# Kernel optimization log

Measured on AMD Instinct MI355X. Metric: run time of the kernel, lower is better.

The kernel has to match this reference:

```python
import jax, jax.numpy as jnp
import numpy as np
import math

B, T = 8, 16
CODE_NUM = 1024
CODE_SIZE = 48
GRAPH_SIZE = 32
HIDDEN = 150      # hidden_size == t_output_size
T_ATTN = 32       # t_attention_size
DP_ATTN = 32      # DotProductAttention size
OUT = 1024


def _lin(k, fan_in, fan_out):
    s = 1.0 / math.sqrt(fan_in)
    kw, kb = jax.random.split(k)
    W = jax.random.uniform(kw, (fan_in, fan_out), minval=-s, maxval=s, dtype=jnp.float32)
    b = jax.random.uniform(kb, (fan_out,), minval=-s, maxval=s, dtype=jnp.float32)
    return W, b


def setup_inputs():
    key = jax.random.key(0)
    ks = jax.random.split(key, 16)
    u = jax.random.uniform(ks[0], (B, T, CODE_NUM))
    m1 = (u < 0.03).astype(jnp.float32)                   # persistent codes
    m2 = ((u >= 0.03) & (u < 0.05)).astype(jnp.float32)   # emerging neighbor codes
    m3 = ((u >= 0.05) & (u < 0.06)).astype(jnp.float32)   # emerging unrelated codes
    divided = jnp.stack([m1, m2, m3], axis=-1)            # [B,T,N,3], disjoint
    code_x = jnp.clip(m1 + m2 + m3, 0.0, 1.0)             # current-visit codes
    neighbors = ((u >= 0.06) & (u < 0.12)).astype(jnp.float32)
    lens = jax.random.randint(ks[1], (B,), T // 2, T + 1)
    a = (jax.random.uniform(ks[2], (CODE_NUM, CODE_NUM)) < 0.01).astype(jnp.float32)
    adj = a / (a.sum(axis=1, keepdims=True) + 1e-6)
    c_emb = jax.random.normal(ks[3], (CODE_NUM, CODE_SIZE)) * 0.05
    n_emb = jax.random.normal(ks[4], (CODE_NUM, CODE_SIZE)) * 0.05
    u_emb = jax.random.normal(ks[5], (CODE_NUM, GRAPH_SIZE)) * 0.05
    Wg, bg = _lin(ks[6], CODE_SIZE, GRAPH_SIZE)           # GraphLayer dense
    Wi, bi = _lin(ks[7], GRAPH_SIZE, 3 * HIDDEN)          # GRUCell input (r|z|n)
    Wh, bh = _lin(ks[8], HIDDEN, 3 * HIDDEN)              # GRUCell hidden (r|z|n)
    Wq, bq = _lin(ks[9], GRAPH_SIZE, T_ATTN)
    Wk, bk = _lin(ks[10], GRAPH_SIZE, T_ATTN)
    Wv, bv = _lin(ks[11], GRAPH_SIZE, HIDDEN)
    Wd, bd = _lin(ks[12], HIDDEN, DP_ATTN)                # DotProductAttention dense
    context = jax.random.normal(ks[13], (DP_ATTN,)) * 0.1
    Wc, bc = _lin(ks[14], HIDDEN, OUT)                    # Classifier
    return dict(code_x=code_x, divided=divided, neighbors=neighbors, lens=lens,
                adj=adj, c_emb=c_emb, n_emb=n_emb, u_emb=u_emb, Wg=Wg, bg=bg,
                Wi=Wi, bi=bi, Wh=Wh, bh=bh, Wq=Wq, bq=bq, Wk=Wk, bk=bk,
                Wv=Wv, bv=bv, Wd=Wd, bd=bd, context=context, Wc=Wc, bc=bc)


def _forward(code_x, divided, neighbors, lens, adj, c_emb, n_emb, u_emb,
             Wg, bg, Wi, bi, Wh, bh, Wq, bq, Wk, bk, Wv, bv, Wd, bd, context, Wc, bc):
    Bb, Tt, N = code_x.shape
    H = Wh.shape[0]
    NEG = -1e30
    scale = 1.0 / math.sqrt(Wq.shape[1])

    def step(carry, xs):
        h_prev, no_prev = carry                 # [B,N,H], [B,N,G]
        c_t, d_t, n_t, t_idx = xs               # [B,N], [B,N,3], [B,N], scalar
        c = c_t[..., None]
        nb = n_t[..., None]
        # GraphLayer: masked embeddings + one-hop adjacency aggregation
        ce = c * c_emb                           # [B,N,C]
        ne = nb * n_emb
        adj_ce = jnp.einsum('mn,bnc->bmc', adj, ce)
        adj_ne = jnp.einsum('mn,bnc->bmc', adj, ne)
        co = jax.nn.leaky_relu((ce + c * adj_ce + c * adj_ne) @ Wg + bg)      # [B,N,G]
        no = jax.nn.leaky_relu((ne + nb * adj_ne + nb * adj_ce) @ Wg + bg)

        m1 = d_t[..., 0]; m2 = d_t[..., 1]; m3 = d_t[..., 2]
        # TransitionLayer part 1: GRUCell on persistent (m1) codes; h_new starts at 0
        gi = co @ Wi + bi
        gh = h_prev @ Wh + bh
        i_r, i_z, i_n = jnp.split(gi, 3, axis=-1)
        h_r, h_z, h_n = jnp.split(gh, 3, axis=-1)
        r = jax.nn.sigmoid(i_r + h_r)
        z = jax.nn.sigmoid(i_z + h_z)
        n_g = jnp.tanh(i_n + r * h_n)
        h_m1 = (1.0 - z) * n_g + z * h_prev
        h_new = jnp.where(m1[..., None] > 0, h_m1, 0.0)

        # TransitionLayer part 2: single-head attention over emerging (m2|m3) codes, t>0
        m23 = (m2 + m3) > 0
        qrows = jnp.where(m2[..., None] > 0, no_prev,
                          jnp.where(m3[..., None] > 0, u_emb, 0.0))           # [B,N,G]
        q = qrows @ Wq + bq
        k = co @ Wk + bk
        v = qrows @ Wv + bv
        s = jnp.einsum('bia,bja->bij', q, k) * scale
        s = jnp.where(m23[:, None, :], s, NEG)   # keys restricted to m2|m3 set
        h_m23 = jnp.tanh(jnp.einsum('bij,bjh->bih', jax.nn.softmax(s, axis=-1), v))
        use23 = t_idx > 0
        h_new = jnp.where(jnp.logical_and(use23, m23)[..., None], h_m23, h_new)

        # per-step output: max-pool over each active subset (0 if subset empty)
        om1 = jnp.max(jnp.where(m1[..., None] > 0, h_m1, NEG), axis=1)
        om1 = jnp.where(jnp.any(m1 > 0, axis=1)[:, None], om1, 0.0)
        om23 = jnp.max(jnp.where(m23[..., None], h_m23, NEG), axis=1)
        om23 = jnp.where(jnp.logical_and(use23, jnp.any(m23, axis=1))[:, None], om23, 0.0)
        return (h_new, no), om1 + om23

    h0 = jnp.zeros((Bb, N, H), code_x.dtype)
    no0 = jnp.zeros((Bb, N, Wg.shape[1]), code_x.dtype)
    xs = (jnp.moveaxis(code_x, 1, 0), jnp.moveaxis(divided, 1, 0),
          jnp.moveaxis(neighbors, 1, 0), jnp.arange(Tt))
    _, outs = jax.lax.scan(step, (h0, no0), xs)
    outs = jnp.moveaxis(outs, 0, 1)              # [B,T,H]

    # DotProductAttention over (ragged) visit axis
    vu = (outs @ Wd + bd) @ context              # [B,T]
    tmask = jnp.arange(Tt)[None, :] < lens[:, None]
    score = jax.nn.softmax(jnp.where(tmask, vu, NEG), axis=-1)
    pooled = jnp.einsum('bth,bt->bh', outs, score)
    # Classifier (dropout_rate=0 -> identity) with sigmoid activation
    return jax.nn.sigmoid(pooled @ Wc + bc)


def reference(code_x, divided, neighbors, lens, adj, c_emb, n_emb, u_emb,
              Wg, bg, Wi, bi, Wh, bh, Wq, bq, Wk, bk, Wv, bv, Wd, bd, context, Wc, bc):
    return _forward(code_x, divided, neighbors, lens, adj, c_emb, n_emb, u_emb,
                    Wg, bg, Wi, bi, Wh, bh, Wq, bq, Wk, bk, Wv, bv, Wd, bd,
                    context, Wc, bc)
```

## Files before the change

### kernel.cpp

```cpp
#include <hip/hip_runtime.h>

#define Bq   8
#define Tq   16
#define Nq   1024
#define Cq   48
#define Gq   32
#define Hq   150
#define H3q  450
#define TAq  32
#define OUTq 1024
#define BTq  128
#define NBLK (2 * BTq)

#define NC_CAP 128
#define NM_CAP 64
#define NACT   (2 * NC_CAP)
#define MTILE  16
#define NMH    (NM_CAP / 2)

__device__ __forceinline__ float lrelu(float x){ return x > 0.f ? x : 0.01f * x; }
__device__ __forceinline__ float sigm(float x){ return 1.f / (1.f + expf(-x)); }

__device__ int   g_n1[BTq], g_n23[BTq], g_nchain[BTq], g_nchain2[BTq];
__device__ int   g_list1[BTq][NM_CAP];
__device__ int   g_list23[BTq][NM_CAP];
__device__ int   g_mapc[BTq][Nq];
__device__ int   g_mapn[BTq][Nq];
__device__ int   g_chain[BTq][NM_CAP];
__device__ int   g_chain2[BTq][NM_CAP];
__device__ int   g_cls[BTq][NM_CAP];
__device__ float g_co[BTq][NC_CAP][Gq];
__device__ float g_no[BTq][NC_CAP][Gq];
__device__ float g_hm23[BTq][NM_CAP][Hq];
__device__ float g_om23p2[2][BTq][Hq];
__device__ float g_hm1[BTq][NM_CAP][Hq];
__device__ float g_om1p2[2][BTq][Hq];
__device__ float g_om1c[BTq][Hq];

template<typename T>
__device__ __forceinline__ T gld(const T* p){
    return __hip_atomic_load(p, __ATOMIC_RELAXED, __HIP_MEMORY_SCOPE_AGENT);
}
template<typename T>
__device__ __forceinline__ void gst(T* p, T v){
    __hip_atomic_store(p, v, __ATOMIC_RELAXED, __HIP_MEMORY_SCOPE_AGENT);
}

__device__ unsigned int g_done[NBLK][16];

__device__ __forceinline__ void publish(unsigned int val){
    asm volatile("s_waitcnt vmcnt(0)" ::: "memory");
    __syncthreads();
    if (threadIdx.x == 0)
        __hip_atomic_store(&g_done[blockIdx.x][0], val,
                           __ATOMIC_RELAXED, __HIP_MEMORY_SCOPE_AGENT);
}

__device__ __forceinline__ void spin_ge(int b2, unsigned int tgt){
    while ((int)(__hip_atomic_load(&g_done[b2][0],
                                   __ATOMIC_RELAXED, __HIP_MEMORY_SCOPE_AGENT) - tgt) < 0)
        __builtin_amdgcn_s_sleep(4);
}

__device__ __forceinline__ void gi3(const float* co_row, const float* Wi, const float* bi, int h,
                                    float& gr, float& gz, float& gn){
    gr = bi[h]; gz = bi[Hq + h]; gn = bi[2 * Hq + h];
    #pragma unroll
    for (int g = 0; g < Gq; ++g){
        float c = co_row[g];
        const float* w = Wi + g * H3q + h;
        gr += c * w[0];
        gz += c * w[Hq];
        gn += c * w[2 * Hq];
    }
}

#define WARM(ptr, nfloats) { int nv_ = (nfloats) >> 2; \
    for (int i4_ = blk * 512 + tid; i4_ < nv_; i4_ += NBLK * 512){ \
        float4 v_ = ((const float4*)(ptr))[i4_]; \
        wacc += v_.x + v_.y + v_.z + v_.w; } }

union SharedU {
    struct {
        unsigned char cf[Nq], nf[Nq];
        short lc[NC_CAP], ln[NC_CAP];
        short act[NACT];
        float Wg[Cq][Gq];
        float Pact[NACT][Gq];
        float A[MTILE][NACT];
    } co;
    struct {
        unsigned char f1[Nq], f2[Nq], f3[Nq];
        short l1[NM_CAP], l23[NM_CAP];
        unsigned char wm[NMH];
        float co23[NM_CAP][Gq];
        float qr[NM_CAP][Gq];
        float q[NMH][TAq + 1];
        float k[NM_CAP][TAq + 1];
        float s[NMH][NM_CAP + 1];
        float vv[NM_CAP][Hq];
        float hm[NMH][Hq];
    } mid;
    struct {
        short map1p[Nq], map23p[Nq];
        short l1[NM_CAP];
        unsigned char cls[NM_CAP];
        int   m23l[NM_CAP];
        float co1[NMH][Gq];
        float hb[Hq];
        float ghf[H3q];
        float gi[NMH][H3q];
    } g1;
    struct {
        unsigned char defer[NM_CAP];
        float co[Gq];
        float hb[Hq];
        float ghf[H3q];
        float cmax[Hq];
    } g1b;
    struct {
        int   nch2[Tq];
        float co[Gq];
        float hb[Hq];
        float ghf[H3q];
        float outs[Tq][Hq];
        float wdc[Hq];
        float score[Tq];
        float pooled[Hq];
    } fin;
};

#define CO_PREFETCH(P, kk) { int rbase_ = half + (kk) * 2 * MTILE; \
    int ntile_ = min(MTILE, (total - rbase_ + 1) / 2); int lim_ = ntile_ * total; \
    _Pragma("unroll") for (int u = 0; u < 8; ++u){ int idx_ = tid + u * 512; \
        if (idx_ < lim_){ int ti_ = idx_ / total, j_ = idx_ - ti_ * total; \
            P[u] = adj[(size_t)sh.co.act[rbase_ + 2 * ti_] * Nq + sh.co.act[j_]]; } } }

#define CO_STORE(P, kk) { int rbase_ = half + (kk) * 2 * MTILE; \
    int ntile_ = min(MTILE, (total - rbase_ + 1) / 2); int lim_ = ntile_ * total; \
    _Pragma("unroll") for (int u = 0; u < 8; ++u){ int idx_ = tid + u * 512; \
        if (idx_ < lim_){ int ti_ = idx_ / total, j_ = idx_ - ti_ * total; \
            sh.co.A[ti_][j_] = P[u]; } } }

#define CO_COMPUTE(kk) { int rbase_ = half + (kk) * 2 * MTILE; \
    int ntile_ = min(MTILE, (total - rbase_ + 1) / 2); \
    if (grp < ntile_){ int r_ = rbase_ + 2 * grp; float agg_ = 0.f; \
        _Pragma("unroll 4") for (int j_ = 0; j_ < total; ++j_) \
            agg_ += sh.co.A[grp][j_] * sh.co.Pact[j_][g]; \
        float v_ = lrelu(sh.co.Pact[r_][g] + agg_ + bgv); \
        if (r_ < nc) gst(&g_co[bt][r_][g], v_); else gst(&g_no[bt][r_ - nc][g], v_); } }

__global__ __launch_bounds__(512, 1) void k_fused(
    const float* code_x, const float* divided, const float* neighbors,
    const int* lens, const float* adj, const float* c_emb, const float* n_emb,
    const float* u_emb, const float* Wg, const float* bg,
    const float* Wi, const float* bi, const float* Wh, const float* bh,
    const float* Wq_, const float* bq_, const float* Wk_, const float* bk_,
    const float* Wv_, const float* bv_, const float* Wd, const float* bd,
    const float* ctx, const float* Wc, const float* bc, float* out)
{
    __shared__ SharedU sh;
    __shared__ int s_n0, s_n1v, s_i2;
    const int tid = threadIdx.x;
    const int blk = blockIdx.x;
    const int bt   = blk >> 1;
    const int half = blk & 1;
    const int t    = bt % Tq;
    const int btp  = bt - 1;
    const unsigned int bar0 = __hip_atomic_load(&g_done[blk][0],
                                                __ATOMIC_RELAXED, __HIP_MEMORY_SCOPE_AGENT);

    float wacc = 0.f;
    WARM(adj,     Nq * Nq);
    WARM(divided, BTq * Nq * 3);
    WARM(c_emb,   Nq * Cq);
    WARM(n_emb,   Nq * Cq);
    WARM(u_emb,   Nq * Gq);
    WARM(Wi,      Gq * H3q);
    WARM(Wh,      Hq * H3q);
    WARM(Wc,      Hq * OUTq);
    WARM(Wv_,     Gq * Hq);
    WARM(Wd,      Hq * TAq);

    {
        int wave = tid >> 6, lane = tid & 63;
        for (int n = tid; n < Nq; n += 512){
            sh.co.cf[n] = (code_x[bt * Nq + n]    > 0.f) ? 1 : 0;
            sh.co.nf[n] = (neighbors[bt * Nq + n] > 0.f) ? 1 : 0;
        }
        for (int i = tid; i < Cq * Gq; i += 512) (&sh.co.Wg[0][0])[i] = Wg[i];
        __syncthreads();
        if (wave == 0){
            int base = 0;
            for (int start = 0; start < Nq; start += 64){
                int n = start + lane;
                int pred = sh.co.cf[n];
                unsigned long long mm = __ballot(pred != 0);
                int pos = base + (int)__popcll(mm & ((1ull << lane) - 1ull));
                if (pred && pos < NC_CAP) sh.co.lc[pos] = (short)n;
                base += (int)__popcll(mm);
            }
            if (lane == 0) s_n0 = min(base, NC_CAP);
        } else if (wave == 1){
            int base = 0;
            for (int start = 0; start < Nq; start += 64){
                int n = start + lane;
                int pred = sh.co.nf[n];
                unsigned long long mm = __ballot(pred != 0);
                int pos = base + (int)__popcll(mm & ((1ull << lane) - 1ull));
                if (pred && pos < NC_CAP) sh.co.ln[pos] = (short)n;
                base += (int)__popcll(mm);
            }
            if (lane == 0) s_n1v = min(base, NC_CAP);
        } else {
            if (half == 0) for (int n = tid - 128; n < Nq; n += 384) gst(&g_mapc[bt][n], -1);
            else           for (int n = tid - 128; n < Nq; n += 384) gst(&g_mapn[bt][n], -1);
        }
        __syncthreads();
        int nc = s_n0, nn = s_n1v, total = nc + nn;

        for (int i = tid; i < total; i += 512) sh.co.act[i] = (i < nc) ? sh.co.lc[i] : sh.co.ln[i - nc];
        if (half == 0) for (int i = tid; i < nc; i += 512) gst(&g_mapc[bt][sh.co.lc[i]], i);
        else           for (int i = tid; i < nn; i += 512) gst(&g_mapn[bt][sh.co.ln[i]], i);
        __syncthreads();

        for (int idx = tid; idx < total * Gq; idx += 512){
            int i = idx >> 5, g = idx & 31;
            int row = sh.co.act[i];
            const float* e = (i < nc) ? (c_emb + row * Cq) : (n_emb + row * Cq);
            float acc = 0.f;
            #pragma unroll
            for (int c = 0; c < Cq; ++c) acc += e[c] * sh.co.Wg[c][g];
            sh.co.Pact[i][g] = acc;
        }
        __syncthreads();

        int g = tid & 31, grp = tid >> 5;
        float bgv = bg[g];
        int ntiles = (total > half) ? (total - half + 2 * MTILE - 1) / (2 * MTILE) : 0;
        float pA[8], pB[8];
        if (ntiles > 0) CO_PREFETCH(pA, 0);
        for (int k = 0; k < ntiles; ){
            CO_STORE(pA, k);
            __syncthreads();
            if (k + 1 < ntiles) CO_PREFETCH(pB, k + 1);
            CO_COMPUTE(k);
            __syncthreads();
            ++k; if (k >= ntiles) break;
            CO_STORE(pB, k);
            __syncthreads();
            if (k + 1 < ntiles) CO_PREFETCH(pA, k + 1);
            CO_COMPUTE(k);
            __syncthreads();
            ++k;
        }
    }
    float dv[6];
    #pragma unroll
    for (int u = 0; u < 6; ++u) dv[u] = divided[(size_t)bt * (Nq * 3) + tid + u * 512];
    asm volatile("" :: "v"(wacc));
    publish(bar0 + 1);
    if (tid == 0) spin_ge(blk ^ 1, bar0 + 1);
    else if (t > 0 && tid == 1) spin_ge(2 * btp,     bar0 + 1);
    else if (t > 0 && tid == 2) spin_ge(2 * btp + 1, bar0 + 1);
    __syncthreads();

    {
        int wave = tid >> 6, lane = tid & 63;
        #pragma unroll
        for (int u = 0; u < 6; ++u){
            int idx = tid + u * 512;
            int n = idx / 3, c = idx - n * 3;
            unsigned char f = (dv[u] > 0.f) ? 1 : 0;
            if (c == 0) sh.mid.f1[n] = f;
            else if (c == 1) sh.mid.f2[n] = f;
            else sh.mid.f3[n] = f;
        }
        __syncthreads();
        if (wave == 0){
            int base = 0;
            for (int start = 0; start < Nq; start += 64){
                int n = start + lane;
                int pred = sh.mid.f1[n];
                unsigned long long mm = __ballot(pred != 0);
                int pos = base + (int)__popcll(mm & ((1ull << lane) - 1ull));
                if (pred && pos < NM_CAP) sh.mid.l1[pos] = (short)n;
                base += (int)__popcll(mm);
            }
            if (lane == 0) s_n0 = min(base, NM_CAP);
        } else if (wave == 1){
            int base = 0;
            for (int start = 0; start < Nq; start += 64){
                int n = start + lane;
                int m2 = sh.mid.f2[n], m3 = sh.mid.f3[n];
                int pred = m2 | m3;
                unsigned long long mm = __ballot(pred != 0);
                int pos = base + (int)__popcll(mm & ((1ull << lane) - 1ull));
                if (pred && pos < NM_CAP) sh.mid.l23[pos] = (short)(n | (m2 ? 0x400 : 0));
                base += (int)__popcll(mm);
            }
            if (lane == 0) s_n1v = min(base, NM_CAP);
        }
        __syncthreads();
        int n1 = s_n0, n23 = s_n1v;
        if (half == 0){
            for (int i = tid; i < n1;  i += 512) gst(&g_list1[bt][i],  (int)sh.mid.l1[i]);
            for (int i = tid; i < n23; i += 512) gst(&g_list23[bt][i], (int)sh.mid.l23[i]);
            if (tid == 0){ gst(&g_n1[bt], n1); gst(&g_n23[bt], n23); }
        }
        if (t != 0 && n23 != 0){
            int nMy = (n23 > half) ? ((n23 - half + 1) >> 1) : 0;

            for (int il = tid; il < nMy; il += 512){
                int row = sh.mid.l23[2 * il + half] & 1023;
                unsigned char wmv = 0;
                if (t < Tq - 1) wmv = (divided[((size_t)(bt + 1) * Nq + row) * 3] > 0.f) ? 1 : 0;
                sh.mid.wm[il] = wmv;
            }
            for (int idx = tid; idx < n23 * Gq; idx += 512){
                int i = idx >> 5, g = idx & 31;
                sh.mid.co23[i][g] = gld(&g_co[bt][gld(&g_mapc[bt][sh.mid.l23[i] & 1023])][g]);
            }
            for (int idx = tid; idx < n23 * Gq; idx += 512){
                int i = idx >> 5, g = idx & 31;
                int e = sh.mid.l23[i], row = e & 1023;
                float qv;
                if (e & 0x400){
                    int slot = gld(&g_mapn[btp][row]);
                    qv = (slot >= 0) ? gld(&g_no[btp][slot][g]) : lrelu(bg[g]);
                } else {
                    qv = u_emb[row * Gq + g];
                }
                sh.mid.qr[i][g] = qv;
            }
            __syncthreads();
            for (int idx = tid; idx < n23 * TAq; idx += 512){
                int i = idx >> 5, a = idx & 31;
                float acck = bk_[a];
                #pragma unroll
                for (int g = 0; g < Gq; ++g) acck += sh.mid.co23[i][g] * Wk_[g * TAq + a];
                sh.mid.k[i][a] = acck;
            }
            for (int idx = tid; idx < nMy * TAq; idx += 512){
                int il = idx >> 5, a = idx & 31;
                int i = 2 * il + half;
                float accq = bq_[a];
                #pragma unroll
                for (int g = 0; g < Gq; ++g) accq += sh.mid.qr[i][g] * Wq_[g * TAq + a];
                sh.mid.q[il][a] = accq;
            }
            for (int idx = tid; idx < n23 * Hq; idx += 512){
                int i = idx / Hq, h = idx % Hq;
                float acc = bv_[h];
                #pragma unroll
                for (int g = 0; g < Gq; ++g) acc += sh.mid.qr[i][g] * Wv_[g * Hq + h];
                sh.mid.vv[i][h] = acc;
            }
            __syncthreads();

            const float scale = 0.17677669529663687f;
            for (int idx = tid; idx < nMy * n23; idx += 512){
                int il = idx / n23, j = idx % n23;
                float acc = 0.f;
                #pragma unroll
                for (int a = 0; a < TAq; ++a) acc += sh.mid.q[il][a] * sh.mid.k[j][a];
                sh.mid.s[il][j] = acc * scale;
            }
            __syncthreads();
            for (int il = tid; il < nMy; il += 512){
                float mx = -1e30f;
                for (int j = 0; j < n23; ++j) mx = fmaxf(mx, sh.mid.s[il][j]);
                float sum = 0.f;
                for (int j = 0; j < n23; ++j){ float e = expf(sh.mid.s[il][j] - mx); sh.mid.s[il][j] = e; sum += e; }
                float inv = 1.f / sum;
                for (int j = 0; j < n23; ++j) sh.mid.s[il][j] *= inv;
            }
            __syncthreads();
            for (int idx = tid; idx < nMy * Hq; idx += 512){
                int il = idx / Hq, h = idx % Hq;
                float acc = 0.f;
                for (int j = 0; j < n23; ++j) acc += sh.mid.s[il][j] * sh.mid.vv[j][h];
                sh.mid.hm[il][h] = tanhf(acc);
            }
            __syncthreads();
            for (int idx = tid; idx < nMy * Hq; idx += 512){
                int il = idx / Hq, h = idx % Hq;
                if (sh.mid.wm[il]) gst(&g_hm23[bt][2 * il + half][h], sh.mid.hm[il][h]);
            }
            for (int h = tid; h < Hq; h += 512){
                float mx = -1e30f;
                for (int il = 0; il < nMy; ++il) mx = fmaxf(mx, sh.mid.hm[il][h]);
                gst(&g_om23p2[half][bt][h], mx);
            }
        }
    }
    publish(bar0 + 2);
    if (tid == 0) spin_ge(blk ^ 1, bar0 + 2);
    else if (t > 0 && tid == 1) spin_ge(2 * btp,     bar0 + 2);
    else if (t > 0 && tid == 2) spin_ge(2 * btp + 1, bar0 + 2);
    __syncthreads();

    {
        int n1 = gld(&g_n1[bt]);
        int nMy = (n1 > half) ? ((n1 - half + 1) >> 1) : 0;
        for (int n = tid; n < Nq; n += 512){
            if (t >= 1) sh.g1.map1p[n] = -1;
            if (t >= 2) sh.g1.map23p[n] = -1;
        }
        for (int i = tid; i < n1; i += 512) sh.g1.l1[i] = (short)gld(&g_list1[bt][i]);
        __syncthreads();
        if (t >= 1){
            int n1p = gld(&g_n1[btp]);
            for (int i = tid; i < n1p; i += 512) sh.g1.map1p[gld(&g_list1[btp][i])] = (short)i;
            if (t >= 2){
                int n23p = gld(&g_n23[btp]);
                for (int i = tid; i < n23p; i += 512) sh.g1.map23p[gld(&g_list23[btp][i]) & 1023] = (short)i;
            }
        }
        __syncthreads();
        if (tid < 64){
            int i = tid;
            int cls = 0, sp = -1;
            if (i < n1 && t >= 1){
                int row = sh.g1.l1[i];
                if (sh.g1.map1p[row] >= 0){ cls = 1; sp = sh.g1.map1p[row]; }
                else if (t >= 2 && sh.g1.map23p[row] >= 0){ cls = 2; sp = sh.g1.map23p[row]; }
            }
            if (i < n1) sh.g1.cls[i] = (unsigned char)cls;
            if (half == 0 && i < n1) gst(&g_cls[bt][i], cls);
            unsigned long long mch = __ballot(cls == 1);
            unsigned long long m23 = __ballot(cls == 2 && (i & 1) == half);
            int pch = (int)__popcll(mch & ((1ull << i) - 1ull));
            int p23 = (int)__popcll(m23 & ((1ull << i) - 1ull));
            if (half == 0 && cls == 1) gst(&g_chain[bt][pch], (i << 16) | sp);
            if (cls == 2 && (i & 1) == half) sh.g1.m23l[p23] = (i << 16) | sp;
            if (i == 0){
                s_i2 = (int)__popcll(m23);
                if (half == 0) gst(&g_nchain[bt], (int)__popcll(mch));
            }
        }
        for (int idx = tid; idx < nMy * Gq; idx += 512){
            int il = idx >> 5, g = idx & 31;
            sh.g1.co1[il][g] = gld(&g_co[bt][gld(&g_mapc[bt][sh.g1.l1[2 * il + half]])][g]);
        }
        __syncthreads();

        if (tid < H3q){
            float wcol[Gq];
            #pragma unroll
            for (int g = 0; g < Gq; ++g) wcol[g] = Wi[g * H3q + tid];
            float bij = bi[tid];
            for (int il = 0; il < nMy; ++il){
                float acc = bij;
                #pragma unroll
                for (int g = 0; g < Gq; ++g) acc += sh.g1.co1[il][g] * wcol[g];
                sh.g1.gi[il][tid] = acc;
            }
        }
        __syncthreads();

        for (int idx = tid; idx < nMy * Hq; idx += 512){
            int il = idx / Hq, h = idx % Hq;
            int i = 2 * il + half;
            if (sh.g1.cls[i] != 0) continue;
            float gr = sh.g1.gi[il][h], gz = sh.g1.gi[il][Hq + h], gn = sh.g1.gi[il][2 * Hq + h];
            float r  = sigm(gr + bh[h]);
            float z  = sigm(gz + bh[Hq + h]);
            float ng = tanhf(gn + r * bh[2 * Hq + h]);
            sh.g1.gi[il][h] = (1.f - z) * ng;
        }
        __syncthreads();

        int nf23 = s_i2;
        for (int f = 0; f < nf23; ++f){
            int pk = sh.g1.m23l[f]; int i = pk >> 16, sp = pk & 0xffff;
            int il = i >> 1;
            for (int h = tid; h < Hq; h += 512) sh.g1.hb[h] = gld(&g_hm23[btp][sp][h]);
            __syncthreads();
            for (int j = tid; j < H3q; j += 512){
                float acc = bh[j];
                for (int k2 = 0; k2 < Hq; ++k2) acc += sh.g1.hb[k2] * Wh[k2 * H3q + j];
                sh.g1.ghf[j] = acc;
            }
            __syncthreads();
            for (int h = tid; h < Hq; h += 512){
                float gr = sh.g1.gi[il][h], gz = sh.g1.gi[il][Hq + h], gn = sh.g1.gi[il][2 * Hq + h];
                float r  = sigm(gr + sh.g1.ghf[h]);
                float z  = sigm(gz + sh.g1.ghf[Hq + h]);
                float ng = tanhf(gn + r * sh.g1.ghf[2 * Hq + h]);
                sh.g1.gi[il][h] = (1.f - z) * ng + z * sh.g1.hb[h];
            }
            __syncthreads();
        }

        for (int idx = tid; idx < nMy * Hq; idx += 512){
            int il = idx / Hq, h = idx % Hq;
            int i = 2 * il + half;
            if (sh.g1.cls[i] != 1) gst(&g_hm1[bt][i][h], sh.g1.gi[il][h]);
        }
        for (int h = tid; h < Hq; h += 512){
            float mx = -1e30f;
            for (int il = 0; il < nMy; ++il)
                if (sh.g1.cls[2 * il + half] != 1) mx = fmaxf(mx, sh.g1.gi[il][h]);
            gst(&g_om1p2[half][bt][h], mx);
        }
    }

    if (half == 1){
        publish(bar0 + 5);
        return;
    }
    publish(bar0 + 3);
    if (t > 0){
        if (tid == 0) spin_ge(2 * btp,     bar0 + 3);
        else if (tid == 1) spin_ge(2 * btp + 1, bar0 + 3);
    }
    __syncthreads();

    {
        int nch = (t > 0) ? gld(&g_nchain[bt]) : 0;
        for (int h = tid; h < Hq; h += 512) sh.g1b.cmax[h] = -1e30f;
        if (tid < 64){
            int c = tid;
            int defer = 0;
            if (c < nch){
                int sp = gld(&g_chain[bt][c]) & 0xffff;
                defer = (gld(&g_cls[btp][sp]) == 1) ? 1 : 0;
                sh.g1b.defer[c] = (unsigned char)defer;
            }
            unsigned long long md = __ballot((c < nch) && defer);
            int pos = (int)__popcll(md & ((1ull << c) - 1ull));
            if ((c < nch) && defer) gst(&g_chain2[bt][pos], gld(&g_chain[bt][c]));
            if (c == 0) gst(&g_nchain2[bt], (int)__popcll(md));
        }
        __syncthreads();
        for (int c = 0; c < nch; ++c){
            if (sh.g1b.defer[c]) continue;
            int pk = gld(&g_chain[bt][c]); int i = pk >> 16, sp = pk & 0xffff;
            if (tid < Gq) sh.g1b.co[tid] = gld(&g_co[bt][gld(&g_mapc[bt][gld(&g_list1[bt][i])])][tid]);
            for (int h = tid; h < Hq; h += 512) sh.g1b.hb[h] = gld(&g_hm1[btp][sp][h]);
            __syncthreads();
            for (int j = tid; j < H3q; j += 512){
                float acc = bh[j];
                for (int k2 = 0; k2 < Hq; ++k2) acc += sh.g1b.hb[k2] * Wh[k2 * H3q + j];
                sh.g1b.ghf[j] = acc;
            }
            __syncthreads();
            for (int h = tid; h < Hq; h += 512){
                float gr, gz, gn;
                gi3(sh.g1b.co, Wi, bi, h, gr, gz, gn);
                float r  = sigm(gr + sh.g1b.ghf[h]);
                float z  = sigm(gz + sh.g1b.ghf[Hq + h]);
                float ng = tanhf(gn + r * sh.g1b.ghf[2 * Hq + h]);
                float v  = (1.f - z) * ng + z * sh.g1b.hb[h];
                gst(&g_hm1[bt][i][h], v);
                sh.g1b.cmax[h] = fmaxf(sh.g1b.cmax[h], v);
            }
            __syncthreads();
        }
        for (int h = tid; h < Hq; h += 512) gst(&g_om1c[bt][h], sh.g1b.cmax[h]);
    }

    if ((blk & 31) != 0){
        publish(bar0 + 5);
        return;
    }
    publish(bar0 + 4);
    {
        int b = blk >> 5;
        if (tid < 32){
            int tt = tid >> 1, par = tid & 1;
            spin_ge(32 * b + 2 * tt + par, par ? (bar0 + 3) : (bar0 + 4));
        }
    }
    __syncthreads();

    {
        int b = blk >> 5;
        if (tid < Tq) sh.fin.nch2[tid] = (tid > 0) ? gld(&g_nchain2[b * Tq + tid]) : 0;
        __syncthreads();
        for (int tt = 1; tt < Tq; ++tt){
            int bt2 = b * Tq + tt, btp2 = bt2 - 1;
            int nch2 = sh.fin.nch2[tt];
            for (int c = 0; c < nch2; ++c){
                int pk = gld(&g_chain2[bt2][c]); int i = pk >> 16, sp = pk & 0xffff;
                if (tid < Gq) sh.fin.co[tid] = gld(&g_co[bt2][gld(&g_mapc[bt2][gld(&g_list1[bt2][i])])][tid]);
                for (int h = tid; h < Hq; h += 512) sh.fin.hb[h] = gld(&g_hm1[btp2][sp][h]);
                __syncthreads();
                for (int j = tid; j < H3q; j += 512){
                    float acc = bh[j];
                    for (int k2 = 0; k2 < Hq; ++k2) acc += sh.fin.hb[k2] * Wh[k2 * H3q + j];
                    sh.fin.ghf[j] = acc;
                }
                __syncthreads();
                for (int h = tid; h < Hq; h += 512){
                    float gr, gz, gn;
                    gi3(sh.fin.co, Wi, bi, h, gr, gz, gn);
                    float r  = sigm(gr + sh.fin.ghf[h]);
                    float z  = sigm(gz + sh.fin.ghf[Hq + h]);
                    float ng = tanhf(gn + r * sh.fin.ghf[2 * Hq + h]);
                    gst(&g_hm1[bt2][i][h], (1.f - z) * ng + z * sh.fin.hb[h]);
                }
                __syncthreads();
            }
        }
        for (int idx = tid; idx < Tq * Hq; idx += 512){
            int tt = idx / Hq, h = idx % Hq;
            int bt2 = b * Tq + tt;
            int n1 = gld(&g_n1[bt2]), n23 = (tt > 0) ? gld(&g_n23[bt2]) : 0;
            float o = 0.f;
            if (n1 > 0){
                float mx = fmaxf(fmaxf(gld(&g_om1p2[0][bt2][h]), gld(&g_om1p2[1][bt2][h])),
                                 gld(&g_om1c[bt2][h]));
                int nd = sh.fin.nch2[tt];
                for (int c = 0; c < nd; ++c){
                    int i = gld(&g_chain2[bt2][c]) >> 16;
                    mx = fmaxf(mx, gld(&g_hm1[bt2][i][h]));
                }
                o = mx;
            }
            if (n23 > 0) o += fmaxf(gld(&g_om23p2[0][bt2][h]), gld(&g_om23p2[1][bt2][h]));
            sh.fin.outs[tt][h] = o;
        }
        for (int h = tid; h < Hq; h += 512){
            float acc = 0.f;
            for (int d = 0; d < 32; ++d) acc += Wd[h * 32 + d] * ctx[d];
            sh.fin.wdc[h] = acc;
        }
        __syncthreads();
        int len = lens[b];
        if (tid < Tq){
            int tt = tid;
            float acc = 0.f;
            for (int d = 0; d < 32; ++d) acc += bd[d] * ctx[d];
            for (int h = 0; h < Hq; ++h) acc += sh.fin.outs[tt][h] * sh.fin.wdc[h];
            sh.fin.score[tt] = (tt < len) ? acc : -1e30f;
        }
        __syncthreads();
        if (tid == 0){
            float mx = -1e30f;
            for (int tt = 0; tt < Tq; ++tt) mx = fmaxf(mx, sh.fin.score[tt]);
            float sum = 0.f;
            for (int tt = 0; tt < Tq; ++tt){ float e = expf(sh.fin.score[tt] - mx); sh.fin.score[tt] = e; sum += e; }
            float inv = 1.f / sum;
            for (int tt = 0; tt < Tq; ++tt) sh.fin.score[tt] *= inv;
        }
        __syncthreads();
        for (int h = tid; h < Hq; h += 512){
            float acc = 0.f;
            for (int tt = 0; tt < Tq; ++tt) acc += sh.fin.score[tt] * sh.fin.outs[tt][h];
            sh.fin.pooled[h] = acc;
        }
        __syncthreads();
        for (int o = tid; o < OUTq; o += 512){
            float acc = bc[o];
            for (int h = 0; h < Hq; ++h) acc += sh.fin.pooled[h] * Wc[h * OUTq + o];
            out[b * OUTq + o] = sigm(acc);
        }
    }
    publish(bar0 + 5);
}

extern "C" void kernel_launch(void* const* d_in, const int* in_sizes, int n_in,
                              void* d_out, int out_size, void* d_ws, size_t ws_size,
                              hipStream_t stream){
    const float* code_x    = (const float*)d_in[0];
    const float* divided   = (const float*)d_in[1];
    const float* neighbors = (const float*)d_in[2];
    const int*   lens      = (const int*)  d_in[3];
    const float* adj       = (const float*)d_in[4];
    const float* c_emb     = (const float*)d_in[5];
    const float* n_emb     = (const float*)d_in[6];
    const float* u_emb     = (const float*)d_in[7];
    const float* Wg        = (const float*)d_in[8];
    const float* bg        = (const float*)d_in[9];
    const float* Wi        = (const float*)d_in[10];
    const float* bi        = (const float*)d_in[11];
    const float* Wh        = (const float*)d_in[12];
    const float* bh        = (const float*)d_in[13];
    const float* Wq_       = (const float*)d_in[14];
    const float* bq_       = (const float*)d_in[15];
    const float* Wk_       = (const float*)d_in[16];
    const float* bk_       = (const float*)d_in[17];
    const float* Wv_       = (const float*)d_in[18];
    const float* bv_       = (const float*)d_in[19];
    const float* Wd_       = (const float*)d_in[20];
    const float* bd_       = (const float*)d_in[21];
    const float* ctx       = (const float*)d_in[22];
    const float* Wc_       = (const float*)d_in[23];
    const float* bc_       = (const float*)d_in[24];
    float* out = (float*)d_out;

    hipLaunchKernelGGL(k_fused, dim3(NBLK), dim3(512), 0, stream,
                       code_x, divided, neighbors, lens, adj, c_emb, n_emb, u_emb,
                       Wg, bg, Wi, bi, Wh, bh, Wq_, bq_, Wk_, bk_, Wv_, bv_,
                       Wd_, bd_, ctx, Wc_, bc_, out);
}
```

Baseline: 243.3 us.

## Double block size to 1024 threads and batch GRU chain updates in chunks

Raises the thread count per block from 512 to 1024 and doubles the co-occurrence row tile (MTILE 16→32), rescaling every strided loop to match. The sequential per-chain GRU loop in the g1b phase becomes chunked processing of up to 16 non-deferred chains at once, with a separate max reduction, which cuts the number of block-wide barriers. The Wi projection is split across two threads per column. This raises register and LDS pressure and could lower occupancy or break assumptions that were tied to 512 threads, such as the divided indexing.

```diff
diff --git a/kernel.cpp b/kernel.cpp
--- a/kernel.cpp
+++ b/kernel.cpp
@@ -11,12 +11,14 @@
 #define OUTq 1024
 #define BTq  128
 #define NBLK (2 * BTq)
+#define THREADS 1024
 
 #define NC_CAP 128
 #define NM_CAP 64
 #define NACT   (2 * NC_CAP)
-#define MTILE  16
+#define MTILE  32
 #define NMH    (NM_CAP / 2)
+#define CHUNK  16
 
 __device__ __forceinline__ float lrelu(float x){ return x > 0.f ? x : 0.01f * x; }
 __device__ __forceinline__ float sigm(float x){ return 1.f / (1.f + expf(-x)); }
@@ -76,7 +78,7 @@
 }
 
 #define WARM(ptr, nfloats) { int nv_ = (nfloats) >> 2; \
-    for (int i4_ = blk * 512 + tid; i4_ < nv_; i4_ += NBLK * 512){ \
+    for (int i4_ = blk * THREADS + tid; i4_ < nv_; i4_ += NBLK * THREADS){ \
         float4 v_ = ((const float4*)(ptr))[i4_]; \
         wacc += v_.x + v_.y + v_.z + v_.w; } }
 
@@ -112,10 +114,11 @@
         float gi[NMH][H3q];
     } g1;
     struct {
-        unsigned char defer[NM_CAP];
-        float co[Gq];
-        float hb[Hq];
-        float ghf[H3q];
+        int   proc[NM_CAP];
+        float hb[CHUNK][Hq];
+        float co[CHUNK][Gq];
+        float ghf[CHUNK][H3q];
+        float hm[CHUNK][Hq];
         float cmax[Hq];
     } g1b;
     struct {
@@ -132,13 +135,13 @@
 
 #define CO_PREFETCH(P, kk) { int rbase_ = half + (kk) * 2 * MTILE; \
     int ntile_ = min(MTILE, (total - rbase_ + 1) / 2); int lim_ = ntile_ * total; \
-    _Pragma("unroll") for (int u = 0; u < 8; ++u){ int idx_ = tid + u * 512; \
+    _Pragma("unroll") for (int u = 0; u < 8; ++u){ int idx_ = tid + u * THREADS; \
         if (idx_ < lim_){ int ti_ = idx_ / total, j_ = idx_ - ti_ * total; \
             P[u] = adj[(size_t)sh.co.act[rbase_ + 2 * ti_] * Nq + sh.co.act[j_]]; } } }
 
 #define CO_STORE(P, kk) { int rbase_ = half + (kk) * 2 * MTILE; \
     int ntile_ = min(MTILE, (total - rbase_ + 1) / 2); int lim_ = ntile_ * total; \
-    _Pragma("unroll") for (int u = 0; u < 8; ++u){ int idx_ = tid + u * 512; \
+    _Pragma("unroll") for (int u = 0; u < 8; ++u){ int idx_ = tid + u * THREADS; \
         if (idx_ < lim_){ int ti_ = idx_ / total, j_ = idx_ - ti_ * total; \
             sh.co.A[ti_][j_] = P[u]; } } }
 
@@ -150,7 +153,7 @@
         float v_ = lrelu(sh.co.Pact[r_][g] + agg_ + bgv); \
         if (r_ < nc) gst(&g_co[bt][r_][g], v_); else gst(&g_no[bt][r_ - nc][g], v_); } }
 
-__global__ __launch_bounds__(512, 1) void k_fused(
+__global__ __launch_bounds__(THREADS, 1) void k_fused(
     const float* code_x, const float* divided, const float* neighbors,
     const int* lens, const float* adj, const float* c_emb, const float* n_emb,
     const float* u_emb, const float* Wg, const float* bg,
@@ -184,11 +187,11 @@
 
     {
         int wave = tid >> 6, lane = tid & 63;
-        for (int n = tid; n < Nq; n += 512){
+        for (int n = tid; n < Nq; n += THREADS){
             sh.co.cf[n] = (code_x[bt * Nq + n]    > 0.f) ? 1 : 0;
             sh.co.nf[n] = (neighbors[bt * Nq + n] > 0.f) ? 1 : 0;
         }
-        for (int i = tid; i < Cq * Gq; i += 512) (&sh.co.Wg[0][0])[i] = Wg[i];
+        for (int i = tid; i < Cq * Gq; i += THREADS) (&sh.co.Wg[0][0])[i] = Wg[i];
         __syncthreads();
         if (wave == 0){
             int base = 0;
@@ -213,18 +216,18 @@
             }
             if (lane == 0) s_n1v = min(base, NC_CAP);
         } else {
-            if (half == 0) for (int n = tid - 128; n < Nq; n += 384) gst(&g_mapc[bt][n], -1);
-            else           for (int n = tid - 128; n < Nq; n += 384) gst(&g_mapn[bt][n], -1);
+            if (half == 0) for (int n = tid - 128; n < Nq; n += 896) gst(&g_mapc[bt][n], -1);
+            else           for (int n = tid - 128; n < Nq; n += 896) gst(&g_mapn[bt][n], -1);
         }
         __syncthreads();
         int nc = s_n0, nn = s_n1v, total = nc + nn;
 
-        for (int i = tid; i < total; i += 512) sh.co.act[i] = (i < nc) ? sh.co.lc[i] : sh.co.ln[i - nc];
-        if (half == 0) for (int i = tid; i < nc; i += 512) gst(&g_mapc[bt][sh.co.lc[i]], i);
-        else           for (int i = tid; i < nn; i += 512) gst(&g_mapn[bt][sh.co.ln[i]], i);
-        __syncthreads();
-
-        for (int idx = tid; idx < total * Gq; idx += 512){
+        for (int i = tid; i < total; i += THREADS) sh.co.act[i] = (i < nc) ? sh.co.lc[i] : sh.co.ln[i - nc];
+        if (half == 0) for (int i = tid; i < nc; i += THREADS) gst(&g_mapc[bt][sh.co.lc[i]], i);
+        else           for (int i = tid; i < nn; i += THREADS) gst(&g_mapn[bt][sh.co.ln[i]], i);
+        __syncthreads();
+
+        for (int idx = tid; idx < total * Gq; idx += THREADS){
             int i = idx >> 5, g = idx & 31;
             int row = sh.co.act[i];
             const float* e = (i < nc) ? (c_emb + row * Cq) : (n_emb + row * Cq);
@@ -255,9 +258,9 @@
             ++k;
         }
     }
-    float dv[6];
+    float dv[3];
     #pragma unroll
-    for (int u = 0; u < 6; ++u) dv[u] = divided[(size_t)bt * (Nq * 3) + tid + u * 512];
+    for (int u = 0; u < 3; ++u) dv[u] = divided[(size_t)bt * (Nq * 3) + tid + u * THREADS];
     asm volatile("" :: "v"(wacc));
     publish(bar0 + 1);
     if (tid == 0) spin_ge(blk ^ 1, bar0 + 1);
@@ -268,8 +271,8 @@
     {
         int wave = tid >> 6, lane = tid & 63;
         #pragma unroll
-        for (int u = 0; u < 6; ++u){
-            int idx = tid + u * 512;
+        for (int u = 0; u < 3; ++u){
+            int idx = tid + u * THREADS;
             int n = idx / 3, c = idx - n * 3;
             unsigned char f = (dv[u] > 0.f) ? 1 : 0;
             if (c == 0) sh.mid.f1[n] = f;
@@ -304,24 +307,24 @@
         __syncthreads();
         int n1 = s_n0, n23 = s_n1v;
         if (half == 0){
-            for (int i = tid; i < n1;  i += 512) gst(&g_list1[bt][i],  (int)sh.mid.l1[i]);
-            for (int i = tid; i < n23; i += 512) gst(&g_list23[bt][i], (int)sh.mid.l23[i]);
+            for (int i = tid; i < n1;  i += THREADS) gst(&g_list1[bt][i],  (int)sh.mid.l1[i]);
+            for (int i = tid; i < n23; i += THREADS) gst(&g_list23[bt][i], (int)sh.mid.l23[i]);
             if (tid == 0){ gst(&g_n1[bt], n1); gst(&g_n23[bt], n23); }
         }
         if (t != 0 && n23 != 0){
             int nMy = (n23 > half) ? ((n23 - half + 1) >> 1) : 0;
 
-            for (int il = tid; il < nMy; il += 512){
+            for (int il = tid; il < nMy; il += THREADS){
                 int row = sh.mid.l23[2 * il + half] & 1023;
                 unsigned char wmv = 0;
                 if (t < Tq - 1) wmv = (divided[((size_t)(bt + 1) * Nq + row) * 3] > 0.f) ? 1 : 0;
                 sh.mid.wm[il] = wmv;
             }
-            for (int idx = tid; idx < n23 * Gq; idx += 512){
+            for (int idx = tid; idx < n23 * Gq; idx += THREADS){
                 int i = idx >> 5, g = idx & 31;
                 sh.mid.co23[i][g] = gld(&g_co[bt][gld(&g_mapc[bt][sh.mid.l23[i] & 1023])][g]);
             }
-            for (int idx = tid; idx < n23 * Gq; idx += 512){
+            for (int idx = tid; idx < n23 * Gq; idx += THREADS){
                 int i = idx >> 5, g = idx & 31;
                 int e = sh.mid.l23[i], row = e & 1023;
                 float qv;
@@ -334,14 +337,14 @@
                 sh.mid.qr[i][g] = qv;
             }
             __syncthreads();
-            for (int idx = tid; idx < n23 * TAq; idx += 512){
+            for (int idx = tid; idx < n23 * TAq; idx += THREADS){
                 int i = idx >> 5, a = idx & 31;
                 float acck = bk_[a];
                 #pragma unroll
                 for (int g = 0; g < Gq; ++g) acck += sh.mid.co23[i][g] * Wk_[g * TAq + a];
                 sh.mid.k[i][a] = acck;
             }
-            for (int idx = tid; idx < nMy * TAq; idx += 512){
+            for (int idx = tid; idx < nMy * TAq; idx += THREADS){
                 int il = idx >> 5, a = idx & 31;
                 int i = 2 * il + half;
                 float accq = bq_[a];
@@ -349,7 +352,7 @@
                 for (int g = 0; g < Gq; ++g) accq += sh.mid.qr[i][g] * Wq_[g * TAq + a];
                 sh.mid.q[il][a] = accq;
             }
-            for (int idx = tid; idx < n23 * Hq; idx += 512){
+            for (int idx = tid; idx < n23 * Hq; idx += THREADS){
                 int i = idx / Hq, h = idx % Hq;
                 float acc = bv_[h];
                 #pragma unroll
@@ -359,7 +362,7 @@
             __syncthreads();
 
             const float scale = 0.17677669529663687f;
-            for (int idx = tid; idx < nMy * n23; idx += 512){
+            for (int idx = tid; idx < nMy * n23; idx += THREADS){
                 int il = idx / n23, j = idx % n23;
                 float acc = 0.f;
                 #pragma unroll
@@ -367,7 +370,7 @@
                 sh.mid.s[il][j] = acc * scale;
             }
             __syncthreads();
-            for (int il = tid; il < nMy; il += 512){
+            for (int il = tid; il < nMy; il += THREADS){
                 float mx = -1e30f;
                 for (int j = 0; j < n23; ++j) mx = fmaxf(mx, sh.mid.s[il][j]);
                 float sum = 0.f;
@@ -376,18 +379,18 @@
                 for (int j = 0; j < n23; ++j) sh.mid.s[il][j] *= inv;
             }
             __syncthreads();
-            for (int idx = tid; idx < nMy * Hq; idx += 512){
+            for (int idx = tid; idx < nMy * Hq; idx += THREADS){
                 int il = idx / Hq, h = idx % Hq;
                 float acc = 0.f;
                 for (int j = 0; j < n23; ++j) acc += sh.mid.s[il][j] * sh.mid.vv[j][h];
                 sh.mid.hm[il][h] = tanhf(acc);
             }
             __syncthreads();
-            for (int idx = tid; idx < nMy * Hq; idx += 512){
+            for (int idx = tid; idx < nMy * Hq; idx += THREADS){
                 int il = idx / Hq, h = idx % Hq;
                 if (sh.mid.wm[il]) gst(&g_hm23[bt][2 * il + half][h], sh.mid.hm[il][h]);
             }
-            for (int h = tid; h < Hq; h += 512){
+            for (int h = tid; h < Hq; h += THREADS){
                 float mx = -1e30f;
                 for (int il = 0; il < nMy; ++il) mx = fmaxf(mx, sh.mid.hm[il][h]);
                 gst(&g_om23p2[half][bt][h], mx);
@@ -403,18 +406,18 @@
     {
         int n1 = gld(&g_n1[bt]);
         int nMy = (n1 > half) ? ((n1 - half + 1) >> 1) : 0;
-        for (int n = tid; n < Nq; n += 512){
+        for (int n = tid; n < Nq; n += THREADS){
             if (t >= 1) sh.g1.map1p[n] = -1;
             if (t >= 2) sh.g1.map23p[n] = -1;
         }
-        for (int i = tid; i < n1; i += 512) sh.g1.l1[i] = (short)gld(&g_list1[bt][i]);
+        for (int i = tid; i < n1; i += THREADS) sh.g1.l1[i] = (short)gld(&g_list1[bt][i]);
         __syncthreads();
         if (t >= 1){
             int n1p = gld(&g_n1[btp]);
-            for (int i = tid; i < n1p; i += 512) sh.g1.map1p[gld(&g_list1[btp][i])] = (short)i;
+            for (int i = tid; i < n1p; i += THREADS) sh.g1.map1p[gld(&g_list1[btp][i])] = (short)i;
             if (t >= 2){
                 int n23p = gld(&g_n23[btp]);
-                for (int i = tid; i < n23p; i += 512) sh.g1.map23p[gld(&g_list23[btp][i]) & 1023] = (short)i;
+                for (int i = tid; i < n23p; i += THREADS) sh.g1.map23p[gld(&g_list23[btp][i]) & 1023] = (short)i;
             }
         }
         __syncthreads();
@@ -439,27 +442,28 @@
                 if (half == 0) gst(&g_nchain[bt], (int)__popcll(mch));
             }
         }
-        for (int idx = tid; idx < nMy * Gq; idx += 512){
+        for (int idx = tid; idx < nMy * Gq; idx += THREADS){
             int il = idx >> 5, g = idx & 31;
             sh.g1.co1[il][g] = gld(&g_co[bt][gld(&g_mapc[bt][sh.g1.l1[2 * il + half]])][g]);
         }
         __syncthreads();
 
-        if (tid < H3q){
+        if (tid < 2 * H3q){
+            int j = tid >> 1, p = tid & 1;
             float wcol[Gq];
             #pragma unroll
-            for (int g = 0; g < Gq; ++g) wcol[g] = Wi[g * H3q + tid];
-            float bij = bi[tid];
-            for (int il = 0; il < nMy; ++il){
+            for (int g = 0; g < Gq; ++g) wcol[g] = Wi[g * H3q + j];
+            float bij = bi[j];
+            for (int il = p; il < nMy; il += 2){
                 float acc = bij;
                 #pragma unroll
                 for (int g = 0; g < Gq; ++g) acc += sh.g1.co1[il][g] * wcol[g];
-                sh.g1.gi[il][tid] = acc;
-            }
-        }
-        __syncthreads();
-
-        for (int idx = tid; idx < nMy * Hq; idx += 512){
+                sh.g1.gi[il][j] = acc;
+            }
+        }
+        __syncthreads();
+
+        for (int idx = tid; idx < nMy * Hq; idx += THREADS){
             int il = idx / Hq, h = idx % Hq;
             int i = 2 * il + half;
             if (sh.g1.cls[i] != 0) continue;
@@ -475,15 +479,15 @@
         for (int f = 0; f < nf23; ++f){
             int pk = sh.g1.m23l[f]; int i = pk >> 16, sp = pk & 0xffff;
             int il = i >> 1;
-            for (int h = tid; h < Hq; h += 512) sh.g1.hb[h] = gld(&g_hm23[btp][sp][h]);
-            __syncthreads();
-            for (int j = tid; j < H3q; j += 512){
+            for (int h = tid; h < Hq; h += THREADS) sh.g1.hb[h] = gld(&g_hm23[btp][sp][h]);
+            __syncthreads();
+            for (int j = tid; j < H3q; j += THREADS){
                 float acc = bh[j];
                 for (int k2 = 0; k2 < Hq; ++k2) acc += sh.g1.hb[k2] * Wh[k2 * H3q + j];
                 sh.g1.ghf[j] = acc;
             }
             __syncthreads();
-            for (int h = tid; h < Hq; h += 512){
+            for (int h = tid; h < Hq; h += THREADS){
                 float gr = sh.g1.gi[il][h], gz = sh.g1.gi[il][Hq + h], gn = sh.g1.gi[il][2 * Hq + h];
                 float r  = sigm(gr + sh.g1.ghf[h]);
                 float z  = sigm(gz + sh.g1.ghf[Hq + h]);
@@ -493,12 +497,12 @@
             __syncthreads();
         }
 
-        for (int idx = tid; idx < nMy * Hq; idx += 512){
+        for (int idx = tid; idx < nMy * Hq; idx += THREADS){
             int il = idx / Hq, h = idx % Hq;
             int i = 2 * il + half;
             if (sh.g1.cls[i] != 1) gst(&g_hm1[bt][i][h], sh.g1.gi[il][h]);
         }
-        for (int h = tid; h < Hq; h += 512){
+        for (int h = tid; h < Hq; h += THREADS){
             float mx = -1e30f;
             for (int il = 0; il < nMy; ++il)
                 if (sh.g1.cls[2 * il + half] != 1) mx = fmaxf(mx, sh.g1.gi[il][h]);
@@ -519,46 +523,69 @@
 
     {
         int nch = (t > 0) ? gld(&g_nchain[bt]) : 0;
-        for (int h = tid; h < Hq; h += 512) sh.g1b.cmax[h] = -1e30f;
+        for (int h = tid; h < Hq; h += THREADS) sh.g1b.cmax[h] = -1e30f;
         if (tid < 64){
             int c = tid;
-            int defer = 0;
+            int pk = 0, defer = 0;
             if (c < nch){
-                int sp = gld(&g_chain[bt][c]) & 0xffff;
+                pk = gld(&g_chain[bt][c]);
+                int sp = pk & 0xffff;
                 defer = (gld(&g_cls[btp][sp]) == 1) ? 1 : 0;
-                sh.g1b.defer[c] = (unsigned char)defer;
             }
             unsigned long long md = __ballot((c < nch) && defer);
-            int pos = (int)__popcll(md & ((1ull << c) - 1ull));
-            if ((c < nch) && defer) gst(&g_chain2[bt][pos], gld(&g_chain[bt][c]));
-            if (c == 0) gst(&g_nchain2[bt], (int)__popcll(md));
-        }
-        __syncthreads();
-        for (int c = 0; c < nch; ++c){
-            if (sh.g1b.defer[c]) continue;
-            int pk = gld(&g_chain[bt][c]); int i = pk >> 16, sp = pk & 0xffff;
-            if (tid < Gq) sh.g1b.co[tid] = gld(&g_co[bt][gld(&g_mapc[bt][gld(&g_list1[bt][i])])][tid]);
-            for (int h = tid; h < Hq; h += 512) sh.g1b.hb[h] = gld(&g_hm1[btp][sp][h]);
-            __syncthreads();
-            for (int j = tid; j < H3q; j += 512){
+            unsigned long long mp = __ballot((c < nch) && !defer);
+            int pos  = (int)__popcll(md & ((1ull << c) - 1ull));
+            int ppos = (int)__popcll(mp & ((1ull << c) - 1ull));
+            if ((c < nch) && defer)  gst(&g_chain2[bt][pos], pk);
+            if ((c < nch) && !defer) sh.g1b.proc[ppos] = pk;
+            if (c == 0){
+                gst(&g_nchain2[bt], (int)__popcll(md));
+                s_i2 = (int)__popcll(mp);
+            }
+        }
+        __syncthreads();
+        int nproc = s_i2;
+        for (int cb = 0; cb < nproc; cb += CHUNK){
+            int nc2 = min(CHUNK, nproc - cb);
+            for (int idx = tid; idx < nc2 * Hq; idx += THREADS){
+                int c = idx / Hq, h = idx % Hq;
+                int sp = sh.g1b.proc[cb + c] & 0xffff;
+                sh.g1b.hb[c][h] = gld(&g_hm1[btp][sp][h]);
+            }
+            for (int idx = tid; idx < nc2 * Gq; idx += THREADS){
+                int c = idx >> 5, g = idx & 31;
+                int i = sh.g1b.proc[cb + c] >> 16;
+                sh.g1b.co[c][g] = gld(&g_co[bt][gld(&g_mapc[bt][gld(&g_list1[bt][i])])][g]);
+            }
+            __syncthreads();
+            for (int idx = tid; idx < nc2 * H3q; idx += THREADS){
+                int c = idx / H3q, j = idx - c * H3q;
                 float acc = bh[j];
-                for (int k2 = 0; k2 < Hq; ++k2) acc += sh.g1b.hb[k2] * Wh[k2 * H3q + j];
-                sh.g1b.ghf[j] = acc;
-            }
-            __syncthreads();
-            for (int h = tid; h < Hq; h += 512){
+                for (int k2 = 0; k2 < Hq; ++k2) acc += sh.g1b.hb[c][k2] * Wh[k2 * H3q + j];
+                sh.g1b.ghf[c][j] = acc;
+            }
+            __syncthreads();
+            for (int idx = tid; idx < nc2 * Hq; idx += THREADS){
+                int c = idx / Hq, h = idx % Hq;
+                int i = sh.g1b.proc[cb + c] >> 16;
                 float gr, gz, gn;
-                gi3(sh.g1b.co, Wi, bi, h, gr, gz, gn);
-                float r  = sigm(gr + sh.g1b.ghf[h]);
-                float z  = sigm(gz + sh.g1b.ghf[Hq + h]);
-                float ng = tanhf(gn + r * sh.g1b.ghf[2 * Hq + h]);
-                float v  = (1.f - z) * ng + z * sh.g1b.hb[h];
+                gi3(sh.g1b.co[c], Wi, bi, h, gr, gz, gn);
+                float r  = sigm(gr + sh.g1b.ghf[c][h]);
+                float z  = sigm(gz + sh.g1b.ghf[c][Hq + h]);
+                float ng = tanhf(gn + r * sh.g1b.ghf[c][2 * Hq + h]);
+                float v  = (1.f - z) * ng + z * sh.g1b.hb[c][h];
                 gst(&g_hm1[bt][i][h], v);
-                sh.g1b.cmax[h] = fmaxf(sh.g1b.cmax[h], v);
-            }
-            __syncthreads();
-        }
-        for (int h = tid; h < Hq; h += 512) gst(&g_om1c[bt][h], sh.g1b.cmax[h]);
+                sh.g1b.hm[c][h] = v;
+            }
+            __syncthreads();
+            for (int h = tid; h < Hq; h += THREADS){
+                float mx = sh.g1b.cmax[h];
+                for (int c = 0; c < nc2; ++c) mx = fmaxf(mx, sh.g1b.hm[c][h]);
+                sh.g1b.cmax[h] = mx;
+            }
+            __syncthreads();
+        }
+        for (int h = tid; h < Hq; h += THREADS) gst(&g_om1c[bt][h], sh.g1b.cmax[h]);
     }
 
     if ((blk & 31) != 0){
@@ -585,15 +612,15 @@
             for (int c = 0; c < nch2; ++c){
                 int pk = gld(&g_chain2[bt2][c]); int i = pk >> 16, sp = pk & 0xffff;
                 if (tid < Gq) sh.fin.co[tid] = gld(&g_co[bt2][gld(&g_mapc[bt2][gld(&g_list1[bt2][i])])][tid]);
-                for (int h = tid; h < Hq; h += 512) sh.fin.hb[h] = gld(&g_hm1[btp2][sp][h]);
+                for (int h = tid; h < Hq; h += THREADS) sh.fin.hb[h] = gld(&g_hm1[btp2][sp][h]);
                 __syncthreads();
-                for (int j = tid; j < H3q; j += 512){
+                for (int j = tid; j < H3q; j += THREADS){
                     float acc = bh[j];
                     for (int k2 = 0; k2 < Hq; ++k2) acc += sh.fin.hb[k2] * Wh[k2 * H3q + j];
                     sh.fin.ghf[j] = acc;
                 }
                 __syncthreads();
-                for (int h = tid; h < Hq; h += 512){
+                for (int h = tid; h < Hq; h += THREADS){
                     float gr, gz, gn;
                     gi3(sh.fin.co, Wi, bi, h, gr, gz, gn);
                     float r  = sigm(gr + sh.fin.ghf[h]);
@@ -604,7 +631,7 @@
                 __syncthreads();
             }
         }
-        for (int idx = tid; idx < Tq * Hq; idx += 512){
+        for (int idx = tid; idx < Tq * Hq; idx += THREADS){
             int tt = idx / Hq, h = idx % Hq;
             int bt2 = b * Tq + tt;
             int n1 = gld(&g_n1[bt2]), n23 = (tt > 0) ? gld(&g_n23[bt2]) : 0;
@@ -622,7 +649,7 @@
             if (n23 > 0) o += fmaxf(gld(&g_om23p2[0][bt2][h]), gld(&g_om23p2[1][bt2][h]));
             sh.fin.outs[tt][h] = o;
         }
-        for (int h = tid; h < Hq; h += 512){
+        for (int h = tid; h < Hq; h += THREADS){
             float acc = 0.f;
             for (int d = 0; d < 32; ++d) acc += Wd[h * 32 + d] * ctx[d];
             sh.fin.wdc[h] = acc;
@@ -646,13 +673,13 @@
             for (int tt = 0; tt < Tq; ++tt) sh.fin.score[tt] *= inv;
         }
         __syncthreads();
-        for (int h = tid; h < Hq; h += 512){
+        for (int h = tid; h < Hq; h += THREADS){
             float acc = 0.f;
             for (int tt = 0; tt < Tq; ++tt) acc += sh.fin.score[tt] * sh.fin.outs[tt][h];
             sh.fin.pooled[h] = acc;
         }
         __syncthreads();
-        for (int o = tid; o < OUTq; o += 512){
+        for (int o = tid; o < OUTq; o += THREADS){
             float acc = bc[o];
             for (int h = 0; h < Hq; ++h) acc += sh.fin.pooled[h] * Wc[h * OUTq + o];
             out[b * OUTq + o] = sigm(acc);
@@ -691,7 +718,7 @@
     const float* bc_       = (const float*)d_in[24];
     float* out = (float*)d_out;
 
-    hipLaunchKernelGGL(k_fused, dim3(NBLK), dim3(512), 0, stream,
+    hipLaunchKernelGGL(k_fused, dim3(NBLK), dim3(THREADS), 0, stream,
                        code_x, divided, neighbors, lens, adj, c_emb, n_emb, u_emb,
                        Wg, bg, Wi, bi, Wh, bh, Wq_, bq_, Wk_, bk_, Wv_, bv_,
                        Wd_, bd_, ctx, Wc_, bc_, out);
```

Measured after the change: 311.4 us. 28.0% more time.
